# Optimization experiments

Measured on AMD Instinct MI355X. Metric: run time of the kernel, lower is better.

## Reference

```python
import jax, jax.numpy as jnp
import numpy as np

N_HEAD = 16


def setup_inputs() -> dict:
    key = jax.random.key(0)
    k1, k2, k3 = jax.random.split(key, 3)
    B, T, C = 2, 2048, 1024
    x = jax.random.normal(k1, (B, T, C), dtype=jnp.float32)
    w_attn = jax.random.normal(k2, (C, 3 * C), dtype=jnp.float32) * 0.02
    w_proj = jax.random.normal(k3, (C, C), dtype=jnp.float32) * 0.02
    return {"x": x, "w_attn": w_attn, "w_proj": w_proj}


def reference(x, w_attn, w_proj):
    B, T, C = x.shape
    H = N_HEAD
    D = C // H
    qkv = x @ w_attn  # [B, T, 3C]
    q, k, v = jnp.split(qkv, 3, axis=2)
    q = q.reshape(B, T, H, D)
    k = k.reshape(B, T, H, D)
    v = v.reshape(B, T, H, D)
    scale = 1.0 / jnp.sqrt(jnp.asarray(D, dtype=x.dtype))
    # Full T x T score matrix, matching the 'standard_attention' path.
    att = jnp.einsum('bthd,bshd->bhts', q, k) * scale  # [B, H, T, T]
    causal = jnp.tril(jnp.ones((T, T), dtype=bool))
    att = jnp.where(causal[None, None, :, :], att, jnp.asarray(-jnp.inf, dtype=att.dtype))
    att = jax.nn.softmax(att, axis=-1)
    # dropout_p is False (== 0.0) in the original module, so no dropout applied.
    y = jnp.einsum('bhts,bshd->bthd', att, v)  # [B, T, H, D]
    y = y.reshape(B, T, C)
    return y @ w_proj
```

## Files before the change

kernel.cpp:

```cpp
#include <hip/hip_runtime.h>
#include <hip/hip_bf16.h>
#include <math.h>

#define BB 2
#define TT 2048
#define HH 16
#define DD 64
#define CC 1024
#define C3 3072

typedef __attribute__((ext_vector_type(8))) short bf16x8;
typedef __attribute__((ext_vector_type(4))) short bf16x4;
typedef __attribute__((ext_vector_type(4))) float f32x4;
typedef __attribute__((ext_vector_type(2))) unsigned int u32x2;

__device__ __forceinline__ unsigned short f2bf(float f) {
  union { float f; unsigned u; } v; v.f = f;
  unsigned r = v.u + 0x7fffu + ((v.u >> 16) & 1u);
  return (unsigned short)(r >> 16);
}
__device__ __forceinline__ unsigned pack2bf(float a, float b) {
  __hip_bfloat162 h = __float22bfloat162_rn(make_float2(a, b));
  union { __hip_bfloat162 h; unsigned u; } cv; cv.h = h;
  return cv.u;
}

__device__ __forceinline__ void async_cp16(const void* g, void* l) {
  __builtin_amdgcn_global_load_lds(
      (const __attribute__((address_space(1))) void*)g,
      (__attribute__((address_space(3))) void*)l, 16, 0, 0);
}

__global__ __launch_bounds__(256)
void prep(const float* __restrict__ x, const float* __restrict__ w_attn,
          const float* __restrict__ w_proj, unsigned short* __restrict__ xb,
          unsigned short* __restrict__ wat, unsigned short* __restrict__ wpt) {
  __shared__ __align__(16) float Ts[64][68];
  const int bx = blockIdx.x, tid = threadIdx.x;
  if (bx < 1024) {
    int i = bx * 256 + tid;
#pragma unroll
    for (int it = 0; it < 4; ++it, i += 262144) {
      const float4 v = ((const float4*)x)[i];
      bf16x4 o = {(short)f2bf(v.x), (short)f2bf(v.y),
                  (short)f2bf(v.z), (short)f2bf(v.w)};
      ((bf16x4*)xb)[i] = o;
    }
    return;
  }
  const float* W;
  unsigned short* WT;
  int Nd, bound, n0, k0;
  float s;
  if (bx < 1792) {
    const int bid = bx - 1024;
    W = w_attn; WT = wat; Nd = 3072; bound = 1024; s = 0.18033688f;
    n0 = (bid % 48) * 64; k0 = (bid / 48) * 64;
  } else {
    const int bid = bx - 1792;
    W = w_proj; WT = wpt; Nd = 1024; bound = 0; s = 1.0f;
    n0 = (bid % 16) * 64; k0 = (bid / 16) * 64;
  }
  const int rl = tid >> 4, c4 = tid & 15;
#pragma unroll
  for (int it = 0; it < 4; ++it) {
    const int r = it * 16 + rl;
    *(float4*)&Ts[r][c4 * 4] =
        *(const float4*)(W + (size_t)(k0 + r) * Nd + n0 + c4 * 4);
  }
  __syncthreads();
#pragma unroll
  for (int it = 0; it < 4; ++it) {
    const int n = it * 16 + rl;
    const float sc = (n0 + n < bound) ? s : 1.0f;
    bf16x4 o = {(short)f2bf(Ts[c4 * 4 + 0][n] * sc),
                (short)f2bf(Ts[c4 * 4 + 1][n] * sc),
                (short)f2bf(Ts[c4 * 4 + 2][n] * sc),
                (short)f2bf(Ts[c4 * 4 + 3][n] * sc)};
    *(bf16x4*)(WT + (size_t)(n0 + n) * CC + k0 + c4 * 4) = o;
  }
}

__global__ __launch_bounds__(256, 3)
void gemm_qkv(const unsigned short* __restrict__ A,
              const unsigned short* __restrict__ BT,
              unsigned short* __restrict__ Cb,
              unsigned short* __restrict__ Vout) {
  __shared__ __align__(16) unsigned short As[2 * 128 * 32];
  __shared__ __align__(16) unsigned short Bs[2 * 128 * 32];

  const int tid = threadIdx.x;
  const int w = tid >> 6, lane = tid & 63;
  const int l15 = lane & 15, quad = lane >> 4;
  const int wm = w >> 1, wn = w & 1;
  const int row0 = blockIdx.y * 128, col0 = blockIdx.x * 128;

  const int ca0 = tid, ca1 = tid + 256;
  const int ra0 = ca0 >> 2, ka0 = ((ca0 & 3) ^ ((ca0 >> 3) & 3)) * 8;
  const int ra1 = ca1 >> 2, ka1 = ((ca1 & 3) ^ ((ca1 >> 3) & 3)) * 8;
  const unsigned short* gA0 = A + (size_t)(row0 + ra0) * CC + ka0;
  const unsigned short* gA1 = A + (size_t)(row0 + ra1) * CC + ka1;
  const unsigned short* gB0 = BT + (size_t)(col0 + ra0) * CC + ka0;
  const unsigned short* gB1 = BT + (size_t)(col0 + ra1) * CC + ka1;
  const int la0 = tid * 16, la1 = tid * 16 + 4096;

  const int fro = l15 * 64 + 16 * (quad ^ ((l15 >> 1) & 3));

  f32x4 acc[4][4];
#pragma unroll
  for (int i = 0; i < 4; ++i)
#pragma unroll
    for (int j = 0; j < 4; ++j) acc[i][j] = (f32x4){0.f, 0.f, 0.f, 0.f};

  async_cp16(gA0, (char*)As + la0);
  async_cp16(gA1, (char*)As + la1);
  async_cp16(gB0, (char*)Bs + la0);
  async_cp16(gB1, (char*)Bs + la1);

  for (int i = 0; i < 32; ++i) {
    const int cur = i & 1;
    __syncthreads();

    if (i + 1 < 32) {
      const int k1 = (i + 1) * 32;
      const int ab = (cur ^ 1) * 8192;
      async_cp16(gA0 + k1, (char*)As + ab + la0);
      async_cp16(gA1 + k1, (char*)As + ab + la1);
      async_cp16(gB0 + k1, (char*)Bs + ab + la0);
      async_cp16(gB1 + k1, (char*)Bs + ab + la1);
    }

    const char* fA = (const char*)As + cur * 8192 + wm * 4096 + fro;
    const char* fB = (const char*)Bs + cur * 8192 + wn * 4096 + fro;

    bf16x8 af[4], bf[4];
#pragma unroll
    for (int mt = 0; mt < 4; ++mt) af[mt] = *(const bf16x8*)(fA + mt * 1024);
#pragma unroll
    for (int nt = 0; nt < 4; ++nt) bf[nt] = *(const bf16x8*)(fB + nt * 1024);
#pragma unroll
    for (int mt = 0; mt < 4; ++mt)
#pragma unroll
      for (int nt = 0; nt < 4; ++nt)
        acc[mt][nt] = __builtin_amdgcn_mfma_f32_16x16x32_bf16(
            af[mt], bf[nt], acc[mt][nt], 0, 0, 0);
  }

  if (col0 >= 2048) {
#pragma unroll
    for (int mt = 0; mt < 4; ++mt) {
      const int rbase = row0 + wm * 64 + mt * 16 + quad * 4;
      const int bq = rbase >> 11, t0 = rbase & 2047;
#pragma unroll
      for (int nt = 0; nt < 4; ++nt) {
        const int d = col0 + wn * 64 + nt * 16 + l15 - 2048;
        bf16x4 o = {(short)f2bf(acc[mt][nt][0]), (short)f2bf(acc[mt][nt][1]),
                    (short)f2bf(acc[mt][nt][2]), (short)f2bf(acc[mt][nt][3])};
        *(bf16x4*)(Vout + (((size_t)(bq << 10) + d) << 11) + t0) = o;
      }
    }
  } else {
#pragma unroll
    for (int mt = 0; mt < 4; ++mt) {
      const int rbase = row0 + wm * 64 + mt * 16 + quad * 4;
#pragma unroll
      for (int r = 0; r < 4; ++r) {
        unsigned short* cr =
            Cb + (size_t)(rbase + r) * C3 + col0 + wn * 64 + l15;
#pragma unroll
        for (int nt = 0; nt < 4; ++nt) cr[nt * 16] = f2bf(acc[mt][nt][r]);
      }
    }
  }
}

__global__ __launch_bounds__(256, 2)
void gemm_out(const unsigned short* __restrict__ A,
              const unsigned short* __restrict__ BT,
              float* __restrict__ Cf) {
  __shared__ __align__(16) unsigned short As[2 * 64 * 64];
  __shared__ __align__(16) unsigned short Bs[2 * 128 * 64];

  const int tid = threadIdx.x;
  const int w = tid >> 6, lane = tid & 63;
  const int l15 = lane & 15, quad = lane >> 4;
  const int wm = w >> 1, wn = w & 1;
  const int row0 = blockIdx.y * 64, col0 = blockIdx.x * 128;

  const int ca0 = tid, ca1 = tid + 256;
  const int ra0 = ca0 >> 3, ka0 = ((ca0 & 7) ^ ((ca0 >> 3) & 7)) * 8;
  const int ra1 = ca1 >> 3, ka1 = ((ca1 & 7) ^ ((ca1 >> 3) & 7)) * 8;
  const unsigned short* gA0 = A + (size_t)(row0 + ra0) * CC + ka0;
  const unsigned short* gA1 = A + (size_t)(row0 + ra1) * CC + ka1;
  const unsigned short* gB[4];
  int lb[4];
#pragma unroll
  for (int t = 0; t < 4; ++t) {
    const int c = tid + t * 256;
    const int rb = c >> 3, kb = ((c & 7) ^ ((c >> 3) & 7)) * 8;
    gB[t] = BT + (size_t)(col0 + rb) * CC + kb;
    lb[t] = c * 16;
  }
  const int la0 = tid * 16, la1 = tid * 16 + 4096;

  const int fro = l15 * 128 + ((quad ^ (l15 & 7)) << 4);

  f32x4 acc[2][4];
#pragma unroll
  for (int i = 0; i < 2; ++i)
#pragma unroll
    for (int j = 0; j < 4; ++j) acc[i][j] = (f32x4){0.f, 0.f, 0.f, 0.f};

  async_cp16(gA0, (char*)As + la0);
  async_cp16(gA1, (char*)As + la1);
#pragma unroll
  for (int t = 0; t < 4; ++t) async_cp16(gB[t], (char*)Bs + lb[t]);

  for (int i = 0; i < 16; ++i) {
    const int cur = i & 1;
    __syncthreads();

    if (i + 1 < 16) {
      const int k1 = (i + 1) * 64;
      const int ab = (cur ^ 1) * 8192, bb = (cur ^ 1) * 16384;
      async_cp16(gA0 + k1, (char*)As + ab + la0);
      async_cp16(gA1 + k1, (char*)As + ab + la1);
#pragma unroll
      for (int t = 0; t < 4; ++t) async_cp16(gB[t] + k1, (char*)Bs + bb + lb[t]);
    }

    const char* fA = (const char*)As + cur * 8192 + wm * 4096 + fro;
    const char* fB = (const char*)Bs + cur * 16384 + wn * 8192 + fro;

#pragma unroll
    for (int kh = 0; kh < 2; ++kh) {
      const int xo = kh * 64;
      bf16x8 af[2], bf[4];
#pragma unroll
      for (int mt = 0; mt < 2; ++mt)
        af[mt] = *(const bf16x8*)(fA + mt * 2048 + ((fro + xo) & 127) - (fro & 127));
#pragma unroll
      for (int nt = 0; nt < 4; ++nt)
        bf[nt] = *(const bf16x8*)(fB + nt * 2048 + ((fro + xo) & 127) - (fro & 127));
#pragma unroll
      for (int mt = 0; mt < 2; ++mt)
#pragma unroll
        for (int nt = 0; nt < 4; ++nt)
          acc[mt][nt] = __builtin_amdgcn_mfma_f32_16x16x32_bf16(
              af[mt], bf[nt], acc[mt][nt], 0, 0, 0);
    }
  }

#pragma unroll
  for (int mt = 0; mt < 2; ++mt) {
    const int rbase = row0 + wm * 32 + mt * 16 + quad * 4;
#pragma unroll
    for (int r = 0; r < 4; ++r) {
      float* cr = Cf + (size_t)(rbase + r) * CC + col0 + wn * 64 + l15;
#pragma unroll
      for (int nt = 0; nt < 4; ++nt) cr[nt * 16] = acc[mt][nt][r];
    }
  }
}

__global__ __launch_bounds__(512, 4)
void attn_mfma(const unsigned short* __restrict__ qkvb,
               const unsigned short* __restrict__ vt,
               unsigned short* __restrict__ y) {
  const int n = blockIdx.x;
  const int bh = (n & 7) + 8 * ((n >> 3) & 3);
  const int qp = n >> 5;
  const int b = bh >> 4, h = bh & 15;
  const int tid = threadIdx.x;
  const int w = tid >> 6;
  const int lane = tid & 63;
  const int l15 = lane & 15, quad = lane >> 4;
  const int wq = w >> 1, kh2 = w & 1;

  __shared__ __align__(16) char Kb[2 * 8192];
  __shared__ __align__(16) char Vb[2 * 8192];
  __shared__ __align__(16) char PsArena[8 * 2304];
  __shared__ float Red2[4][16];

  char* psw = PsArena + w * 2304;
  const int psrow = l15 * 144;

  const int lr = lane >> 3;
  const int lc = lane & 7;
  const int srcoff = ((lc ^ lr) << 4);
  const char* ksrc = (const char*)qkvb + ((size_t)(b * TT) * C3 + 1024 + h * 64) * 2;
  const char* vsrc = (const char*)vt + ((size_t)(b * HH + h) * DD * TT) * 2;

  const int fro = l15 * 128 + ((quad ^ (l15 & 7)) << 4);
  const int vxor = kh2 << 6;
  const int pfoff = ((((quad >> 1) + l15) & 3) << 5) + ((quad & 1) << 4);
  const int epoff = l15 * 64 + ((quad ^ (l15 & 3)) << 4);

  for (int phase = 0; phase < 2; ++phase) {
    const int qt = phase ? qp : 31 - qp;
    const int nt = qt + 1;
    const int rmin = qt * 64 + wq * 16;
    const int rmax = rmin + 15;
    const int dk = rmax - kh2 * 32;
    const int jl = (dk >= 0) ? (dk >> 6) : -1;

    if (phase) __syncthreads();

    const unsigned short* qrow =
        qkvb + (size_t)(b * TT + rmin + l15) * C3 + h * DD;
    bf16x8 qf0 = *(const bf16x8*)(qrow + quad * 8);
    bf16x8 qf1 = *(const bf16x8*)(qrow + 32 + quad * 8);

    f32x4 O[4];
    float lsum = 0.f;
#pragma unroll
    for (int dt = 0; dt < 4; ++dt) O[dt] = (f32x4){0.f, 0.f, 0.f, 0.f};

    async_cp16(ksrc + (size_t)(w * 8 + lr) * (C3 * 2) + srcoff, Kb + w * 1024);
    async_cp16(vsrc + (size_t)(w * 8 + lr) * (TT * 2) + srcoff, Vb + w * 1024);

    for (int j = 0; j < nt; ++j) {
      const int cur = j & 1;
      __syncthreads();

      if (j + 1 < nt) {
        const int key1 = (j + 1) * 64;
        async_cp16(ksrc + (size_t)(key1 + w * 8 + lr) * (C3 * 2) + srcoff,
                   Kb + (cur ^ 1) * 8192 + w * 1024);
        async_cp16(vsrc + (size_t)(w * 8 + lr) * (TT * 2) + key1 * 2 + srcoff,
                   Vb + (cur ^ 1) * 8192 + w * 1024);
      }

      if (j > jl) continue;

      const char* Kc = Kb + cur * 8192;
      const char* Vc = Vb + cur * 8192;
      const int klo = 64 * j + kh2 * 32;

      f32x4 S[2];
#pragma unroll
      for (int kt = 0; kt < 2; ++kt) {
        const int ct = kh2 * 2 + kt;
        bf16x8 k0 = *(const bf16x8*)(Kc + ct * 2048 + fro);
        bf16x8 k1 = *(const bf16x8*)(Kc + ct * 2048 + (fro ^ 64));
        f32x4 z = (f32x4){-12.f, -12.f, -12.f, -12.f};
        z = __builtin_amdgcn_mfma_f32_16x16x32_bf16(k0, qf0, z, 0, 0, 0);
        z = __builtin_amdgcn_mfma_f32_16x16x32_bf16(k1, qf1, z, 0, 0, 0);
        S[kt] = z;
      }

      if (klo + 31 > rmin) {
#pragma unroll
        for (int kt = 0; kt < 2; ++kt)
#pragma unroll
          for (int r = 0; r < 4; ++r)
            if (klo + kt * 16 + quad * 4 + r > rmin + l15)
              S[kt][r] = -INFINITY;
      }

#pragma unroll
      for (int kt = 0; kt < 2; ++kt) {
        u32x2 d;
        d[0] = pack2bf(__builtin_amdgcn_exp2f(S[kt][0]),
                       __builtin_amdgcn_exp2f(S[kt][1]));
        d[1] = pack2bf(__builtin_amdgcn_exp2f(S[kt][2]),
                       __builtin_amdgcn_exp2f(S[kt][3]));
        lsum += __uint_as_float(d[0] << 16) +
                __uint_as_float(d[0] & 0xffff0000u) +
                __uint_as_float(d[1] << 16) +
                __uint_as_float(d[1] & 0xffff0000u);
        *(u32x2*)(psw + psrow + (((kt + l15) & 3) << 5) + quad * 8) = d;
      }

      const bf16x8 pf = *(const bf16x8*)(psw + psrow + pfoff);
#pragma unroll
      for (int dt = 0; dt < 4; ++dt) {
        bf16x8 vf = *(const bf16x8*)(Vc + dt * 2048 + (fro ^ vxor));
        O[dt] = __builtin_amdgcn_mfma_f32_16x16x32_bf16(vf, pf, O[dt], 0, 0, 0);
      }
    }

    lsum += __shfl_xor(lsum, 16, 64);
    lsum += __shfl_xor(lsum, 32, 64);

    __syncthreads();
    if (kh2) {
      char* rs = PsArena + wq * 4096;
#pragma unroll
      for (int dt = 0; dt < 4; ++dt)
        *(f32x4*)(rs + dt * 1024 + epoff) = O[dt];
      if (quad == 0) Red2[wq][l15] = lsum;
    }
    __syncthreads();
    if (!kh2) {
      const char* rs = PsArena + wq * 4096;
#pragma unroll
      for (int dt = 0; dt < 4; ++dt)
        O[dt] += *(const f32x4*)(rs + dt * 1024 + epoff);
      const float inv = 1.0f / (lsum + Red2[wq][l15]);
      unsigned short* yr =
          y + (size_t)(b * TT + rmin + l15) * CC + h * DD + quad * 4;
#pragma unroll
      for (int dt = 0; dt < 4; ++dt) {
        bf16x4 o = {(short)f2bf(O[dt][0] * inv), (short)f2bf(O[dt][1] * inv),
                    (short)f2bf(O[dt][2] * inv), (short)f2bf(O[dt][3] * inv)};
        *(bf16x4*)(yr + dt * 16) = o;
      }
    }
  }
}

extern "C" void kernel_launch(void* const* d_in, const int* in_sizes, int n_in,
                              void* d_out, int out_size, void* d_ws,
                              size_t ws_size, hipStream_t stream) {
  const float* x      = (const float*)d_in[0];
  const float* w_attn = (const float*)d_in[1];
  const float* w_proj = (const float*)d_in[2];
  float* out = (float*)d_out;

  unsigned short* xb   = (unsigned short*)d_ws;
  unsigned short* wat  = xb + (size_t)4096 * 1024;
  unsigned short* wpt  = wat + (size_t)3072 * 1024;
  unsigned short* qkvb = wpt + (size_t)1024 * 1024;
  unsigned short* vt   = qkvb + (size_t)4096 * 3072;
  unsigned short* yb   = vt + (size_t)BB * HH * DD * TT;

  dim3 blk(256);

  prep<<<2048, blk, 0, stream>>>(x, w_attn, w_proj, xb, wat, wpt);

  gemm_qkv<<<dim3(C3 / 128, (BB * TT) / 128), blk, 0, stream>>>(
      xb, wat, qkvb, vt);

  attn_mfma<<<dim3(512, 1, 1), dim3(512), 0, stream>>>(qkvb, vt, yb);

  gemm_out<<<dim3(CC / 128, (BB * TT) / 64), blk, 0, stream>>>(yb, wpt, out);
}
```

Before: 169.4 us.

## Software-pipeline PV matmul one tile behind QK and exp in attention loop

Restructures the attention key loop so that the P·V MFMAs for the previous tile run while the current tile's QK^T scores are computed and exponentiated. V staging grows from double to triple buffering so the previous tile's V stays resident. The PV MFMA block runs at raised wave priority via s_setprio. This adds 8 KB of LDS per block, which could lower occupancy at 4 blocks per CU, and adds loop-carried state and branches.

Measured after the change: 169.3 us. About the same (-0.0%).

```diff
diff --git a/kernel.cpp b/kernel.cpp
--- a/kernel.cpp
+++ b/kernel.cpp
@@ -278,7 +278,7 @@
   const int wq = w >> 1, kh2 = w & 1;
 
   __shared__ __align__(16) char Kb[2 * 8192];
-  __shared__ __align__(16) char Vb[2 * 8192];
+  __shared__ __align__(16) char Vb[3 * 8192];
   __shared__ __align__(16) char PsArena[8 * 2304];
   __shared__ float Red2[4][16];
 
@@ -319,63 +319,84 @@
     async_cp16(ksrc + (size_t)(w * 8 + lr) * (C3 * 2) + srcoff, Kb + w * 1024);
     async_cp16(vsrc + (size_t)(w * 8 + lr) * (TT * 2) + srcoff, Vb + w * 1024);
 
+    int pend = -1;
     for (int j = 0; j < nt; ++j) {
-      const int cur = j & 1;
       __syncthreads();
 
       if (j + 1 < nt) {
         const int key1 = (j + 1) * 64;
         async_cp16(ksrc + (size_t)(key1 + w * 8 + lr) * (C3 * 2) + srcoff,
-                   Kb + (cur ^ 1) * 8192 + w * 1024);
+                   Kb + ((j + 1) & 1) * 8192 + w * 1024);
         async_cp16(vsrc + (size_t)(w * 8 + lr) * (TT * 2) + key1 * 2 + srcoff,
-                   Vb + (cur ^ 1) * 8192 + w * 1024);
-      }
-
-      if (j > jl) continue;
-
-      const char* Kc = Kb + cur * 8192;
-      const char* Vc = Vb + cur * 8192;
-      const int klo = 64 * j + kh2 * 32;
+                   Vb + ((j + 1) % 3) * 8192 + w * 1024);
+      }
+
+      const bool act = (j <= jl);
+      const bool havep = (pend >= 0);
+
+      bf16x8 pf;
+      if (havep) pf = *(const bf16x8*)(psw + psrow + pfoff);
 
       f32x4 S[2];
-#pragma unroll
-      for (int kt = 0; kt < 2; ++kt) {
-        const int ct = kh2 * 2 + kt;
-        bf16x8 k0 = *(const bf16x8*)(Kc + ct * 2048 + fro);
-        bf16x8 k1 = *(const bf16x8*)(Kc + ct * 2048 + (fro ^ 64));
-        f32x4 z = (f32x4){-12.f, -12.f, -12.f, -12.f};
-        z = __builtin_amdgcn_mfma_f32_16x16x32_bf16(k0, qf0, z, 0, 0, 0);
-        z = __builtin_amdgcn_mfma_f32_16x16x32_bf16(k1, qf1, z, 0, 0, 0);
-        S[kt] = z;
-      }
-
-      if (klo + 31 > rmin) {
-#pragma unroll
-        for (int kt = 0; kt < 2; ++kt)
-#pragma unroll
-          for (int r = 0; r < 4; ++r)
-            if (klo + kt * 16 + quad * 4 + r > rmin + l15)
-              S[kt][r] = -INFINITY;
-      }
-
-#pragma unroll
-      for (int kt = 0; kt < 2; ++kt) {
-        u32x2 d;
-        d[0] = pack2bf(__builtin_amdgcn_exp2f(S[kt][0]),
-                       __builtin_amdgcn_exp2f(S[kt][1]));
-        d[1] = pack2bf(__builtin_amdgcn_exp2f(S[kt][2]),
-                       __builtin_amdgcn_exp2f(S[kt][3]));
-        lsum += __uint_as_float(d[0] << 16) +
-                __uint_as_float(d[0] & 0xffff0000u) +
-                __uint_as_float(d[1] << 16) +
-                __uint_as_float(d[1] & 0xffff0000u);
-        *(u32x2*)(psw + psrow + (((kt + l15) & 3) << 5) + quad * 8) = d;
-      }
-
-      const bf16x8 pf = *(const bf16x8*)(psw + psrow + pfoff);
+      if (act) {
+        const char* Kc = Kb + (j & 1) * 8192;
+        const int klo = 64 * j + kh2 * 32;
+#pragma unroll
+        for (int kt = 0; kt < 2; ++kt) {
+          const int ct = kh2 * 2 + kt;
+          bf16x8 k0 = *(const bf16x8*)(Kc + ct * 2048 + fro);
+          bf16x8 k1 = *(const bf16x8*)(Kc + ct * 2048 + (fro ^ 64));
+          f32x4 z = (f32x4){-12.f, -12.f, -12.f, -12.f};
+          z = __builtin_amdgcn_mfma_f32_16x16x32_bf16(k0, qf0, z, 0, 0, 0);
+          z = __builtin_amdgcn_mfma_f32_16x16x32_bf16(k1, qf1, z, 0, 0, 0);
+          S[kt] = z;
+        }
+        if (klo + 31 > rmin) {
+#pragma unroll
+          for (int kt = 0; kt < 2; ++kt)
+#pragma unroll
+            for (int r = 0; r < 4; ++r)
+              if (klo + kt * 16 + quad * 4 + r > rmin + l15)
+                S[kt][r] = -INFINITY;
+        }
+      }
+
+      if (havep) {
+        const char* Vp = Vb + (pend % 3) * 8192;
+        __builtin_amdgcn_s_setprio(1);
+#pragma unroll
+        for (int dt = 0; dt < 4; ++dt) {
+          bf16x8 vf = *(const bf16x8*)(Vp + dt * 2048 + (fro ^ vxor));
+          O[dt] = __builtin_amdgcn_mfma_f32_16x16x32_bf16(vf, pf, O[dt], 0, 0, 0);
+        }
+        __builtin_amdgcn_s_setprio(0);
+        pend = -1;
+      }
+
+      if (act) {
+#pragma unroll
+        for (int kt = 0; kt < 2; ++kt) {
+          u32x2 d;
+          d[0] = pack2bf(__builtin_amdgcn_exp2f(S[kt][0]),
+                         __builtin_amdgcn_exp2f(S[kt][1]));
+          d[1] = pack2bf(__builtin_amdgcn_exp2f(S[kt][2]),
+                         __builtin_amdgcn_exp2f(S[kt][3]));
+          lsum += __uint_as_float(d[0] << 16) +
+                  __uint_as_float(d[0] & 0xffff0000u) +
+                  __uint_as_float(d[1] << 16) +
+                  __uint_as_float(d[1] & 0xffff0000u);
+          *(u32x2*)(psw + psrow + (((kt + l15) & 3) << 5) + quad * 8) = d;
+        }
+        pend = j;
+      }
+    }
+
+    if (pend >= 0) {
+      bf16x8 pf = *(const bf16x8*)(psw + psrow + pfoff);
+      const char* Vp = Vb + (pend % 3) * 8192;
 #pragma unroll
       for (int dt = 0; dt < 4; ++dt) {
-        bf16x8 vf = *(const bf16x8*)(Vc + dt * 2048 + (fro ^ vxor));
+        bf16x8 vf = *(const bf16x8*)(Vp + dt * 2048 + (fro ^ vxor));
         O[dt] = __builtin_amdgcn_mfma_f32_16x16x32_bf16(vf, pf, O[dt], 0, 0, 0);
       }
     }
```

## Triple-buffer K/V tiles with explicit vmcnt waits in attention loop

Applied to the files above, without the earlier changes.

Moves the attention kernel's K/V LDS staging from double to triple buffering, prefetching two tiles ahead. A partial s_waitcnt vmcnt(2) plus a raw s_barrier replaces the full __syncthreads, so the loads for the next tile can stay in flight while the current tile is computed. In exchange, LDS use grows by 16KB per block, which may lower occupancy at launch_bounds(512,4). Correctness now depends on the vmcnt accounting matching exactly two outstanding async copies per tile.

Measured after the change: 170.2 us. Within noise of the previous version (+0.5%).

```diff
diff --git a/kernel.cpp b/kernel.cpp
--- a/kernel.cpp
+++ b/kernel.cpp
@@ -277,8 +277,8 @@
   const int l15 = lane & 15, quad = lane >> 4;
   const int wq = w >> 1, kh2 = w & 1;
 
-  __shared__ __align__(16) char Kb[2 * 8192];
-  __shared__ __align__(16) char Vb[2 * 8192];
+  __shared__ __align__(16) char Kb[3 * 8192];
+  __shared__ __align__(16) char Vb[3 * 8192];
   __shared__ __align__(16) char PsArena[8 * 2304];
   __shared__ float Red2[4][16];
 
@@ -318,23 +318,37 @@
 
     async_cp16(ksrc + (size_t)(w * 8 + lr) * (C3 * 2) + srcoff, Kb + w * 1024);
     async_cp16(vsrc + (size_t)(w * 8 + lr) * (TT * 2) + srcoff, Vb + w * 1024);
-
+    if (nt > 1) {
+      async_cp16(ksrc + (size_t)(64 + w * 8 + lr) * (C3 * 2) + srcoff,
+                 Kb + 8192 + w * 1024);
+      async_cp16(vsrc + (size_t)(w * 8 + lr) * (TT * 2) + 128 + srcoff,
+                 Vb + 8192 + w * 1024);
+    }
+
+    int bj = 0;
     for (int j = 0; j < nt; ++j) {
-      const int cur = j & 1;
-      __syncthreads();
-
       if (j + 1 < nt) {
-        const int key1 = (j + 1) * 64;
-        async_cp16(ksrc + (size_t)(key1 + w * 8 + lr) * (C3 * 2) + srcoff,
-                   Kb + (cur ^ 1) * 8192 + w * 1024);
-        async_cp16(vsrc + (size_t)(w * 8 + lr) * (TT * 2) + key1 * 2 + srcoff,
-                   Vb + (cur ^ 1) * 8192 + w * 1024);
-      }
+        asm volatile("s_waitcnt vmcnt(2)" ::: "memory");
+      } else {
+        asm volatile("s_waitcnt vmcnt(0)" ::: "memory");
+      }
+      __builtin_amdgcn_s_barrier();
+
+      if (j + 2 < nt) {
+        const int key2 = (j + 2) * 64;
+        const int bs = (bj >= 1) ? bj - 1 : 2;
+        async_cp16(ksrc + (size_t)(key2 + w * 8 + lr) * (C3 * 2) + srcoff,
+                   Kb + bs * 8192 + w * 1024);
+        async_cp16(vsrc + (size_t)(w * 8 + lr) * (TT * 2) + key2 * 2 + srcoff,
+                   Vb + bs * 8192 + w * 1024);
+      }
+      const int bjc = bj;
+      bj = (bj + 1 == 3) ? 0 : bj + 1;
 
       if (j > jl) continue;
 
-      const char* Kc = Kb + cur * 8192;
-      const char* Vc = Vb + cur * 8192;
+      const char* Kc = Kb + bjc * 8192;
+      const char* Vc = Vb + bjc * 8192;
       const int klo = 64 * j + kh2 * 32;
 
       f32x4 S[2];
```
